# Optimization experiments

Hardware: AMD Instinct MI355X
Metric: run time of the kernel (lower is better)

Reference implementation:

```python
import jax, jax.numpy as jnp
import numpy as np

B, L, C, K, NLEV, VOCAB, OUT = 32, 1024, 512, 2, 4, 128, 11


def setup_inputs() -> dict:
    key = jax.random.key(0)
    ks = jax.random.split(key, 8)
    x = jax.random.randint(ks[0], (B, L), 0, VOCAB, dtype=jnp.int32)
    mask = jax.random.randint(ks[1], (B, L), 0, 2).astype(jnp.bool_)
    emb = jax.random.uniform(ks[2], (VOCAB, C), minval=-0.5, maxval=0.5, dtype=jnp.float32)
    w1 = jax.random.normal(ks[3], (NLEV, C, C, K), dtype=jnp.float32) * 0.02
    b1 = jnp.zeros((NLEV, C), dtype=jnp.float32)
    w2 = jax.random.normal(ks[4], (NLEV, C, C, K), dtype=jnp.float32) * 0.02
    b2 = jnp.zeros((NLEV, C), dtype=jnp.float32)
    dec_w = jax.random.uniform(ks[5], (OUT, C), minval=-0.5, maxval=0.5, dtype=jnp.float32)
    dec_b = jnp.zeros((OUT,), dtype=jnp.float32)
    return dict(x=x, mask=mask, emb=emb, w1=w1, b1=b1, w2=w2, b2=b2, dec_w=dec_w, dec_b=dec_b)


def _causal_conv(h, w, b, dilation):
    # h: [B, C, L], w: [Cout, Cin, K]; left-pad (K-1)*d == conv+chomp in TCN
    pad = (w.shape[-1] - 1) * dilation
    out = jax.lax.conv_general_dilated(
        h, w, window_strides=(1,), padding=[(pad, 0)],
        rhs_dilation=(dilation,), dimension_numbers=("NCH", "OIH", "NCH"))
    return out + b[None, :, None]


def reference(x, mask, emb, w1, b1, w2, b2, dec_w, dec_b):
    h = emb[x].transpose(0, 2, 1)  # [B, C, L]
    for i in range(NLEV):  # fixed small number of TCN levels
        d = 2 ** i
        res = h
        h = jax.nn.relu(_causal_conv(h, w1[i], b1[i], d))
        h = jax.nn.relu(_causal_conv(h, w2[i], b2[i], d))
        h = jax.nn.relu(h + res)  # residual (in==out channels -> identity shortcut)
    y = jnp.einsum("bcl,oc->blo", h, dec_w) + dec_b  # [B, L, OUT]
    # mask-gather: original keeps only mask-true positions; zero others (jit-safe)
    return y * mask[..., None].astype(y.dtype)
```

## Files before the change

### kernel.cpp

```cpp
#include <hip/hip_runtime.h>
#include <stdint.h>

#define BB 32
#define LL 1024
#define CC 512
#define NN (BB * LL)
#define NLEVS 4
#define OUTD 11
#define LPAD 8
#define LROWS (LL + LPAD)

typedef __attribute__((ext_vector_type(8))) short bf16x8;
typedef __attribute__((ext_vector_type(4))) float f32x4;

static __device__ __forceinline__ unsigned short f2bf(float f) {
    union { float f; uint32_t u; } v; v.f = f;
    uint32_t u = v.u;
    uint32_t r = (u + 0x7fffu + ((u >> 16) & 1u)) >> 16;
    return (unsigned short)r;
}
static __device__ __forceinline__ float bf2f(unsigned short h) {
    union { uint32_t u; float f; } v; v.u = ((uint32_t)h) << 16;
    return v.f;
}

static __device__ __forceinline__ void llds16(const unsigned short* g, unsigned short* l) {
    __builtin_amdgcn_global_load_lds(
        (const __attribute__((address_space(1))) unsigned int*)g,
        (__attribute__((address_space(3))) unsigned int*)l, 16, 0, 0);
}

__global__ __launch_bounds__(256) void prep_kernel(
    const int* __restrict__ x, const float* __restrict__ emb,
    const float* __restrict__ w1, const float* __restrict__ w2,
    const float* __restrict__ dw,
    unsigned short* __restrict__ Hb0, unsigned short* __restrict__ Hb1,
    unsigned short* __restrict__ WpT, unsigned short* __restrict__ dwp)
{
    int b = blockIdx.x;
    if (b < 16384) {
        int e = b * 256 + threadIdx.x;
        int cv = e >> 19;
        int r = e & 524287;
        int j = r >> 12;
        int co = (r >> 3) & 511;
        int h = r & 7;
        int kidx = j * 8 + h;
        int k = (kidx < 512) ? 1 : 0;
        int ci = kidx & 511;
        int lvl = cv >> 1;
        const float* w = (cv & 1) ? w2 : w1;
        WpT[e] = f2bf(w[(((size_t)(lvl * 512 + co) * 512) + ci) * 2 + k]);
    } else if (b < 24576) {
        int t = (b - 16384) * 256 + threadIdx.x;
        int n = t >> 6;
        int c8 = (t & 63) * 8;
        int idx = x[n];
        const float* src = emb + (size_t)idx * CC + c8;
        float4 v0 = *(const float4*)src;
        float4 v1 = *(const float4*)(src + 4);
        ushort4 a, bb;
        a.x = f2bf(v0.x); a.y = f2bf(v0.y); a.z = f2bf(v0.z); a.w = f2bf(v0.w);
        bb.x = f2bf(v1.x); bb.y = f2bf(v1.y); bb.z = f2bf(v1.z); bb.w = f2bf(v1.w);
        int prow = (n >> 10) * LROWS + LPAD + (n & (LL - 1));
        unsigned short* dst = Hb0 + (size_t)prow * CC + c8;
        *(ushort4*)dst = a;
        *(ushort4*)(dst + 4) = bb;
    } else if (b < 24704) {
        int t = (b - 24576) * 256 + threadIdx.x;
        unsigned short* base = (t >> 14) ? Hb1 : Hb0;
        int rem = t & 16383;
        int p = rem >> 9;
        int q = rem & 511;
        size_t off = (size_t)p * (LROWS * CC) + (size_t)q * 8;
        *(uint4*)(base + off) = (uint4){0u, 0u, 0u, 0u};
    } else {
        int e = (b - 24704) * 256 + threadIdx.x;
        int jb = e >> 7;
        int o = (e >> 3) & 15;
        int j = e & 7;
        dwp[e] = f2bf((o < OUTD) ? dw[o * CC + jb * 8 + j] : 0.f);
    }
}

#define BUFH (17 * 512)
template <bool HAS_RES>
__global__ __launch_bounds__(256, 4) void conv_gemm(
    const unsigned short* __restrict__ Ain, const unsigned short* __restrict__ WpT,
    const float* __restrict__ bias, const unsigned short* __restrict__ resB,
    unsigned short* __restrict__ OutB, int d)
{
    __shared__ unsigned short sA[2 * BUFH];
    __shared__ int s_ready[8];
    __shared__ int s_done[8];

    const int tid = threadIdx.x;
    const int wave = tid >> 6, lane = tid & 63;

    const int bid = blockIdx.x;
    const int xcd = bid & 7;
    const int local = bid >> 3;
    const int cb = local >> 5;
    const int nb = xcd + 8 * (local & 31);
    const int co0 = cb * 128;
    const int n0 = nb * 128;

    const int rbase = (n0 >> 10) * LROWS + LPAD + (n0 & (LL - 1));
    const int wm = (wave >> 1) * 64;
    const int wn = (wave & 1) * 64;
    const int lm = lane & 15, quad = lane >> 4;

    const int r8 = lane >> 3;
    const int c8 = lane & 7;

    if (tid < 8) { s_ready[tid] = 0; s_done[tid] = 0; }
    __syncthreads();

    f32x4 acc[4][4];
#pragma unroll
    for (int i = 0; i < 4; ++i)
#pragma unroll
        for (int j = 0; j < 4; ++j) acc[i][j] = (f32x4){0.f, 0.f, 0.f, 0.f};

    auto issue = [&](int it) {
        const unsigned short* gA =
            Ain + (size_t)(rbase - 8 + r8) * CC + it * 64 + (c8 ^ r8) * 8;
        unsigned short* lbase = sA + (it & 1) * BUFH;
        for (int seg = wave; seg < 17; seg += 4)
            llds16(gA + (size_t)seg * 8 * CC, lbase + seg * 512);
    };
    auto spin4 = [&](int* p) {
        volatile int* vp = (volatile int*)p;
        while (*vp < 4) __builtin_amdgcn_s_sleep(1);
    };

    issue(0);

    for (int it = 0; it < 8; ++it) {
        if (it < 7) {
            if (it >= 1) spin4(&s_done[it - 1]);
            issue(it + 1);
            if (wave == 0) __builtin_amdgcn_s_waitcnt(0xF75);
            else           __builtin_amdgcn_s_waitcnt(0xF74);
        } else {
            __builtin_amdgcn_s_waitcnt(0xF70);
        }
        __asm__ volatile("" ::: "memory");
        if (lane == 0) atomicAdd(&s_ready[it], 1);
        spin4(&s_ready[it]);
        __asm__ volatile("" ::: "memory");

        const unsigned short* buf = sA + (it & 1) * BUFH;
        const int jb0 = it * 8;

        auto loadA = [&](int s, bf16x8* af) {
            const int t = s >> 1, ks = s & 1;
            const int shift = t ? d : 0;
            const int rowoff = 8 - shift + wm;
            const int key = (8 - shift + lm) & 7;
            const int cpos = ((ks * 4 + quad) ^ key);
#pragma unroll
            for (int mt = 0; mt < 4; ++mt)
                af[mt] = *(const bf16x8*)&buf[(rowoff + mt * 16 + lm) * 64 + cpos * 8];
        };
        auto loadB = [&](int s, bf16x8* bf) {
            const int t = s >> 1, ks = s & 1;
            const int jb = t * 64 + jb0 + ks * 4 + quad;
            const unsigned short* bbase = WpT + ((size_t)jb * 512 + co0 + wn + lm) * 8;
#pragma unroll
            for (int nt = 0; nt < 4; ++nt)
                bf[nt] = *(const bf16x8*)(bbase + (size_t)nt * 16 * 8);
        };

        bf16x8 afc[4], bfc[4], afn[4], bfn[4];
        loadA(0, afc);
        loadB(0, bfc);
#pragma unroll
        for (int s = 0; s < 4; ++s) {
            if (s < 3) { loadA(s + 1, afn); loadB(s + 1, bfn); }
#pragma unroll
            for (int mt = 0; mt < 4; ++mt)
#pragma unroll
                for (int nt = 0; nt < 4; ++nt)
                    acc[mt][nt] = __builtin_amdgcn_mfma_f32_16x16x32_bf16(
                        afc[mt], bfc[nt], acc[mt][nt], 0, 0, 0);
            if (s < 3) {
#pragma unroll
                for (int q2 = 0; q2 < 4; ++q2) { afc[q2] = afn[q2]; bfc[q2] = bfn[q2]; }
            }
        }

        __asm__ volatile("" ::: "memory");
        if (lane == 0) atomicAdd(&s_done[it], 1);
    }

    float bv[4];
#pragma unroll
    for (int nt = 0; nt < 4; ++nt) bv[nt] = bias[co0 + wn + nt * 16 + lm];

#pragma unroll
    for (int mt = 0; mt < 4; ++mt) {
        int prow0 = rbase + wm + mt * 16 + quad * 4;
#pragma unroll
        for (int nt = 0; nt < 4; ++nt) {
            int co = co0 + wn + nt * 16 + lm;
#pragma unroll
            for (int r = 0; r < 4; ++r) {
                size_t off = (size_t)(prow0 + r) * CC + co;
                float v = acc[mt][nt][r] + bv[nt];
                v = fmaxf(v, 0.f);
                if (HAS_RES) {
                    v += bf2f(resB[off]);
                    v = fmaxf(v, 0.f);
                }
                OutB[off] = f2bf(v);
            }
        }
    }
}

__global__ __launch_bounds__(256) void decode_kernel(
    const unsigned short* __restrict__ H, const unsigned short* __restrict__ dwp,
    const float* __restrict__ db, const int* __restrict__ mask,
    float* __restrict__ out)
{
    const int wave = threadIdx.x >> 6, lane = threadIdx.x & 63;
    const int lm = lane & 15, quad = lane >> 4;
    const int n0 = blockIdx.x * 64 + wave * 16;
    const int prow = ((n0 + lm) >> 10) * LROWS + LPAD + ((n0 + lm) & (LL - 1));

    f32x4 acc = (f32x4){0.f, 0.f, 0.f, 0.f};
#pragma unroll
    for (int ks = 0; ks < 16; ++ks) {
        bf16x8 af = *(const bf16x8*)&H[(size_t)prow * CC + ks * 32 + quad * 8];
        bf16x8 bf = *(const bf16x8*)&dwp[((size_t)(ks * 4 + quad) * 16 + lm) * 8];
        acc = __builtin_amdgcn_mfma_f32_16x16x32_bf16(af, bf, acc, 0, 0, 0);
    }

    if (lm < OUTD) {
        float bo = db[lm];
#pragma unroll
        for (int r = 0; r < 4; ++r) {
            int n = n0 + quad * 4 + r;
            float v = (mask[n] != 0) ? (acc[r] + bo) : 0.f;
            out[(size_t)n * OUTD + lm] = v;
        }
    }
}

extern "C" void kernel_launch(void* const* d_in, const int* in_sizes, int n_in,
                              void* d_out, int out_size, void* d_ws, size_t ws_size,
                              hipStream_t stream)
{
    const int* x = (const int*)d_in[0];
    const int* mask = (const int*)d_in[1];
    const float* emb = (const float*)d_in[2];
    const float* w1 = (const float*)d_in[3];
    const float* b1 = (const float*)d_in[4];
    const float* w2 = (const float*)d_in[5];
    const float* b2 = (const float*)d_in[6];
    const float* dw = (const float*)d_in[7];
    const float* db = (const float*)d_in[8];
    float* out = (float*)d_out;

    char* ws = (char*)d_ws;
    const size_t HBB = (size_t)BB * LROWS * CC * 2;
    unsigned short* Hb0 = (unsigned short*)ws;
    unsigned short* Hb1 = (unsigned short*)(ws + HBB);
    unsigned short* WpT = (unsigned short*)(ws + 2 * HBB);
    unsigned short* dwp = (unsigned short*)(ws + 2 * HBB + (size_t)NLEVS * 2 * CC * 1024 * 2);

    prep_kernel<<<24736, 256, 0, stream>>>(x, emb, w1, w2, dw, Hb0, Hb1, WpT, dwp);

    const int grid = (CC / 128) * (NN / 128);
    for (int i = 0; i < NLEVS; ++i) {
        int d = 1 << i;
        const unsigned short* W1 = WpT + (size_t)(i * 2 + 0) * CC * 1024;
        const unsigned short* W2 = WpT + (size_t)(i * 2 + 1) * CC * 1024;
        conv_gemm<false><<<grid, 256, 0, stream>>>(Hb0, W1, b1 + i * CC, nullptr, Hb1, d);
        conv_gemm<true><<<grid, 256, 0, stream>>>(Hb1, W2, b2 + i * CC, Hb0, Hb0, d);
    }
    decode_kernel<<<NN / 64, 256, 0, stream>>>(Hb0, dwp, db, mask, out);
}
```

Measured before the change: 393.9 us.

## Replace block-wide spin barriers with per-wave-pair private A buffers

The shared 17-segment A tile is split into one private double-buffered region per wave pair, each holding the 72 rows that pair needs. Each wave now loads the whole pair buffer itself and waits only on its own loads. The four-wave atomic ready/done barrier becomes a single flag handshake with the partner wave. This removes cross-wave stalls at the cost of duplicated global-to-LDS loads, since both waves of a pair load the same data, and slightly more LDS.

```diff
diff --git a/kernel.cpp b/kernel.cpp
--- a/kernel.cpp
+++ b/kernel.cpp
@@ -83,19 +83,20 @@
     }
 }
 
-#define BUFH (17 * 512)
+#define PSEG 9
+#define PBUFH (72 * 64)
 template <bool HAS_RES>
 __global__ __launch_bounds__(256, 4) void conv_gemm(
     const unsigned short* __restrict__ Ain, const unsigned short* __restrict__ WpT,
     const float* __restrict__ bias, const unsigned short* __restrict__ resB,
     unsigned short* __restrict__ OutB, int d)
 {
-    __shared__ unsigned short sA[2 * BUFH];
-    __shared__ int s_ready[8];
-    __shared__ int s_done[8];
+    __shared__ unsigned short sA[2 * 2 * PBUFH];
+    __shared__ int s_flag[4][8];
 
     const int tid = threadIdx.x;
     const int wave = tid >> 6, lane = tid & 63;
+    const int pair = wave >> 1;
 
     const int bid = blockIdx.x;
     const int xcd = bid & 7;
@@ -106,14 +107,14 @@
     const int n0 = nb * 128;
 
     const int rbase = (n0 >> 10) * LROWS + LPAD + (n0 & (LL - 1));
-    const int wm = (wave >> 1) * 64;
+    const int wm = pair * 64;
     const int wn = (wave & 1) * 64;
     const int lm = lane & 15, quad = lane >> 4;
 
     const int r8 = lane >> 3;
     const int c8 = lane & 7;
 
-    if (tid < 8) { s_ready[tid] = 0; s_done[tid] = 0; }
+    if (tid < 32) ((int*)s_flag)[tid] = 0;
     __syncthreads();
 
     f32x4 acc[4][4];
@@ -122,41 +123,40 @@
 #pragma unroll
         for (int j = 0; j < 4; ++j) acc[i][j] = (f32x4){0.f, 0.f, 0.f, 0.f};
 
+    unsigned short* pb = sA + pair * (2 * PBUFH);
+    const unsigned short* gAb =
+        Ain + (size_t)(rbase - 8 + wm + r8) * CC + (c8 ^ r8) * 8;
+
     auto issue = [&](int it) {
-        const unsigned short* gA =
-            Ain + (size_t)(rbase - 8 + r8) * CC + it * 64 + (c8 ^ r8) * 8;
-        unsigned short* lbase = sA + (it & 1) * BUFH;
-        for (int seg = wave; seg < 17; seg += 4)
-            llds16(gA + (size_t)seg * 8 * CC, lbase + seg * 512);
-    };
-    auto spin4 = [&](int* p) {
-        volatile int* vp = (volatile int*)p;
-        while (*vp < 4) __builtin_amdgcn_s_sleep(1);
+        const unsigned short* gA = gAb + it * 64;
+        unsigned short* lb = pb + (it & 1) * PBUFH;
+#pragma unroll
+        for (int seg = 0; seg < PSEG; ++seg)
+            llds16(gA + (size_t)seg * 8 * CC, lb + seg * 512);
     };
 
     issue(0);
 
     for (int it = 0; it < 8; ++it) {
         if (it < 7) {
-            if (it >= 1) spin4(&s_done[it - 1]);
+            if (it >= 1) {
+                volatile int* vp = &s_flag[wave ^ 1][it - 1];
+                while (*vp == 0) __builtin_amdgcn_s_sleep(1);
+            }
             issue(it + 1);
-            if (wave == 0) __builtin_amdgcn_s_waitcnt(0xF75);
-            else           __builtin_amdgcn_s_waitcnt(0xF74);
+            __builtin_amdgcn_s_waitcnt(0xF79);
         } else {
             __builtin_amdgcn_s_waitcnt(0xF70);
         }
         __asm__ volatile("" ::: "memory");
-        if (lane == 0) atomicAdd(&s_ready[it], 1);
-        spin4(&s_ready[it]);
-        __asm__ volatile("" ::: "memory");
-
-        const unsigned short* buf = sA + (it & 1) * BUFH;
+
+        const unsigned short* buf = pb + (it & 1) * PBUFH;
         const int jb0 = it * 8;
 
         auto loadA = [&](int s, bf16x8* af) {
             const int t = s >> 1, ks = s & 1;
             const int shift = t ? d : 0;
-            const int rowoff = 8 - shift + wm;
+            const int rowoff = 8 - shift;
             const int key = (8 - shift + lm) & 7;
             const int cpos = ((ks * 4 + quad) ^ key);
 #pragma unroll
@@ -191,7 +191,7 @@
         }
 
         __asm__ volatile("" ::: "memory");
-        if (lane == 0) atomicAdd(&s_done[it], 1);
+        if (lane == 0) *(volatile int*)&s_flag[wave][it] = 1;
     }
 
     float bv[4];
```

New measurement: 413.4 us. +4.9%, slower.
